# Performance work log

Measured on AMD Instinct MI355X. Metric: run time of the kernel, lower is better.

Reference implementation:

```python
import jax, jax.numpy as jnp
import numpy as np
from jax import lax


def setup_inputs() -> dict:
    key = jax.random.key(0)
    x = jax.random.normal(key, (16, 3, 1024, 1024), dtype=jnp.float32)
    return {"x": x, "kernel_size": 7}


def _box_conv(x, kernel, pad):
    # x: (B,1,H,W), kernel: (1,1,k,k); 'same' spatial conv
    return lax.conv_general_dilated(
        x, kernel,
        window_strides=(1, 1),
        padding=[(pad, pad), (pad, pad)],
        dimension_numbers=("NCHW", "OIHW", "NCHW"),
    )


def reference(x, kernel_size):
    k = kernel_size
    pad = k // 2
    # ConvertToLuminance: for 4D input, x.dim()==4 -> channel mean (not RGB weights)
    lum = jnp.mean(x, axis=1, keepdims=True)  # (B,1,H,W)
    kernel = jnp.ones((1, 1, k, k), dtype=x.dtype) / (k * k)
    mean = _box_conv(lum, kernel, pad)
    sqr_mean = _box_conv(lum * lum, kernel, pad)
    var = sqr_mean - mean * mean
    return var
```

## Files before the change

### kernel.cpp

```cpp
#include <hip/hip_runtime.h>

#define Wd 1024
#define Hd 1024
#define SH 16
#define ITER (SH + 6)

__global__ __launch_bounds__(256, 4)
void lvm_stream(const float* __restrict__ x, float* __restrict__ out) {
    __shared__ __align__(16) float L[2][Wd + 8];

    const int b    = blockIdx.y;
    const int row0 = blockIdx.x * SH;
    const int tid  = threadIdx.x;
    const int c0   = tid * 4;

    const float* x0 = x + (size_t)b * 3 * Hd * Wd;
    const float* x1 = x0 + (size_t)Hd * Wd;
    const float* x2 = x1 + (size_t)Hd * Wd;
    float*       ob = out + (size_t)b * Hd * Wd;

    if (tid < 4) {
        L[0][tid] = 0.f; L[0][Wd + 4 + tid] = 0.f;
        L[1][tid] = 0.f; L[1][Wd + 4 + tid] = 0.f;
    }

    float4 ring1[7], ring2[7];

#pragma unroll
    for (int i = 0; i < ITER; ++i) {
        const int ri = row0 - 3 + i;
        float4 lum4 = make_float4(0.f, 0.f, 0.f, 0.f);
        if (ri >= 0 && ri < Hd) {
            size_t o = (size_t)ri * Wd + c0;
            float4 a = *(const float4*)(x0 + o);
            float4 g = *(const float4*)(x1 + o);
            float4 c = *(const float4*)(x2 + o);
            lum4.x = (a.x + g.x + c.x) * (1.f / 3.f);
            lum4.y = (a.y + g.y + c.y) * (1.f / 3.f);
            lum4.z = (a.z + g.z + c.z) * (1.f / 3.f);
            lum4.w = (a.w + g.w + c.w) * (1.f / 3.f);
        }
        float* Lr = L[i & 1];
        *(float4*)(Lr + 4 + c0) = lum4;
        __syncthreads();

        float4 va = *(const float4*)(Lr + c0);
        float4 vb = *(const float4*)(Lr + c0 + 4);
        float4 vc = *(const float4*)(Lr + c0 + 8);
        float v1 = va.y, v2 = va.z, v3 = va.w;
        float v4 = vb.x, v5 = vb.y, v6 = vb.z, v7 = vb.w;
        float v8 = vc.x, v9 = vc.y, v10 = vc.z;

        float s1a = v1 + v2 + v3 + v4 + v5 + v6 + v7;
        float s1b = s1a - v1 + v8;
        float s1c = s1b - v2 + v9;
        float s1d = s1c - v3 + v10;

        float q1 = v1 * v1, q2 = v2 * v2, q3 = v3 * v3, q4 = v4 * v4;
        float q5 = v5 * v5, q6 = v6 * v6, q7 = v7 * v7, q8 = v8 * v8;
        float q9 = v9 * v9, q10 = v10 * v10;
        float s2a = q1 + q2 + q3 + q4 + q5 + q6 + q7;
        float s2b = s2a - q1 + q8;
        float s2c = s2b - q2 + q9;
        float s2d = s2c - q3 + q10;

        ring1[i % 7] = make_float4(s1a, s1b, s1c, s1d);
        ring2[i % 7] = make_float4(s2a, s2b, s2c, s2d);

        if (i >= 6) {
            float4 t1 = ring1[0], t2 = ring2[0];
#pragma unroll
            for (int k = 1; k < 7; ++k) {
                t1.x += ring1[k].x; t1.y += ring1[k].y;
                t1.z += ring1[k].z; t1.w += ring1[k].w;
                t2.x += ring2[k].x; t2.y += ring2[k].y;
                t2.z += ring2[k].z; t2.w += ring2[k].w;
            }
            const float inv = 1.f / 49.f;
            float4 r;
            float mx = t1.x * inv, my = t1.y * inv, mz = t1.z * inv, mw = t1.w * inv;
            r.x = t2.x * inv - mx * mx;
            r.y = t2.y * inv - my * my;
            r.z = t2.z * inv - mz * mz;
            r.w = t2.w * inv - mw * mw;
            const int ro = row0 + i - 6;
            *(float4*)(ob + (size_t)ro * Wd + c0) = r;
        }
    }
}

extern "C" void kernel_launch(void* const* d_in, const int* in_sizes, int n_in,
                              void* d_out, int out_size, void* d_ws, size_t ws_size,
                              hipStream_t stream) {
    const float* x = (const float*)d_in[0];
    float* out = (float*)d_out;
    dim3 grid(Hd / SH, 16);
    lvm_stream<<<grid, dim3(256), 0, stream>>>(x, out);
}
```

Before: 301.9 us.

## Replace LDS halo exchange with wavefront shuffles and double row strip height

Horizontal neighbors now come from wavefront shuffles instead of a shared-memory row buffer, which removes the per-row __syncthreads barrier. Wavefront edge lanes reload the adjacent float4 from global memory to fill the halo. The strip height grows from 16 to 32 rows, cutting redundant halo-row reads, and output stores become nontemporal. The trade-offs are extra global loads at wave boundaries, more unrolled code, and half as many blocks.

```diff
diff --git a/kernel.cpp b/kernel.cpp
--- a/kernel.cpp
+++ b/kernel.cpp
@@ -1,17 +1,27 @@
 #include <hip/hip_runtime.h>
+
+typedef float f4 __attribute__((ext_vector_type(4)));
 
 #define Wd 1024
 #define Hd 1024
-#define SH 16
+#define SH 32
 #define ITER (SH + 6)
+
+__device__ __forceinline__ f4 load_lum(const float* __restrict__ x0,
+                                       const float* __restrict__ x1,
+                                       const float* __restrict__ x2, size_t o) {
+    f4 a = *(const f4*)(x0 + o);
+    f4 g = *(const f4*)(x1 + o);
+    f4 c = *(const f4*)(x2 + o);
+    return (a + g + c) * (1.f / 3.f);
+}
 
 __global__ __launch_bounds__(256, 4)
 void lvm_stream(const float* __restrict__ x, float* __restrict__ out) {
-    __shared__ __align__(16) float L[2][Wd + 8];
-
     const int b    = blockIdx.y;
     const int row0 = blockIdx.x * SH;
     const int tid  = threadIdx.x;
+    const int lane = tid & 63;
     const int c0   = tid * 4;
 
     const float* x0 = x + (size_t)b * 3 * Hd * Wd;
@@ -19,37 +29,38 @@
     const float* x2 = x1 + (size_t)Hd * Wd;
     float*       ob = out + (size_t)b * Hd * Wd;
 
-    if (tid < 4) {
-        L[0][tid] = 0.f; L[0][Wd + 4 + tid] = 0.f;
-        L[1][tid] = 0.f; L[1][Wd + 4 + tid] = 0.f;
-    }
-
-    float4 ring1[7], ring2[7];
+    f4 ring1[7], ring2[7];
 
 #pragma unroll
     for (int i = 0; i < ITER; ++i) {
         const int ri = row0 - 3 + i;
-        float4 lum4 = make_float4(0.f, 0.f, 0.f, 0.f);
-        if (ri >= 0 && ri < Hd) {
-            size_t o = (size_t)ri * Wd + c0;
-            float4 a = *(const float4*)(x0 + o);
-            float4 g = *(const float4*)(x1 + o);
-            float4 c = *(const float4*)(x2 + o);
-            lum4.x = (a.x + g.x + c.x) * (1.f / 3.f);
-            lum4.y = (a.y + g.y + c.y) * (1.f / 3.f);
-            lum4.z = (a.z + g.z + c.z) * (1.f / 3.f);
-            lum4.w = (a.w + g.w + c.w) * (1.f / 3.f);
+        const bool rv = (ri >= 0) && (ri < Hd);
+        f4 lum = {0.f, 0.f, 0.f, 0.f};
+        if (rv) lum = load_lum(x0, x1, x2, (size_t)ri * Wd + c0);
+
+        float v1  = __shfl_up(lum.y, 1);
+        float v2  = __shfl_up(lum.z, 1);
+        float v3  = __shfl_up(lum.w, 1);
+        float v8  = __shfl_down(lum.x, 1);
+        float v9  = __shfl_down(lum.y, 1);
+        float v10 = __shfl_down(lum.z, 1);
+
+        if (lane == 0) {
+            v1 = v2 = v3 = 0.f;
+            if (rv && c0 >= 4) {
+                f4 e = load_lum(x0, x1, x2, (size_t)ri * Wd + (c0 - 4));
+                v1 = e.y; v2 = e.z; v3 = e.w;
+            }
         }
-        float* Lr = L[i & 1];
-        *(float4*)(Lr + 4 + c0) = lum4;
-        __syncthreads();
+        if (lane == 63) {
+            v8 = v9 = v10 = 0.f;
+            if (rv && (c0 + 4) < Wd) {
+                f4 e = load_lum(x0, x1, x2, (size_t)ri * Wd + (c0 + 4));
+                v8 = e.x; v9 = e.y; v10 = e.z;
+            }
+        }
 
-        float4 va = *(const float4*)(Lr + c0);
-        float4 vb = *(const float4*)(Lr + c0 + 4);
-        float4 vc = *(const float4*)(Lr + c0 + 8);
-        float v1 = va.y, v2 = va.z, v3 = va.w;
-        float v4 = vb.x, v5 = vb.y, v6 = vb.z, v7 = vb.w;
-        float v8 = vc.x, v9 = vc.y, v10 = vc.z;
+        const float v4 = lum.x, v5 = lum.y, v6 = lum.z, v7 = lum.w;
 
         float s1a = v1 + v2 + v3 + v4 + v5 + v6 + v7;
         float s1b = s1a - v1 + v8;
@@ -64,27 +75,18 @@
         float s2c = s2b - q2 + q9;
         float s2d = s2c - q3 + q10;
 
-        ring1[i % 7] = make_float4(s1a, s1b, s1c, s1d);
-        ring2[i % 7] = make_float4(s2a, s2b, s2c, s2d);
+        ring1[i % 7] = (f4){s1a, s1b, s1c, s1d};
+        ring2[i % 7] = (f4){s2a, s2b, s2c, s2d};
 
         if (i >= 6) {
-            float4 t1 = ring1[0], t2 = ring2[0];
+            f4 t1 = ring1[0], t2 = ring2[0];
 #pragma unroll
-            for (int k = 1; k < 7; ++k) {
-                t1.x += ring1[k].x; t1.y += ring1[k].y;
-                t1.z += ring1[k].z; t1.w += ring1[k].w;
-                t2.x += ring2[k].x; t2.y += ring2[k].y;
-                t2.z += ring2[k].z; t2.w += ring2[k].w;
-            }
+            for (int k = 1; k < 7; ++k) { t1 += ring1[k]; t2 += ring2[k]; }
             const float inv = 1.f / 49.f;
-            float4 r;
-            float mx = t1.x * inv, my = t1.y * inv, mz = t1.z * inv, mw = t1.w * inv;
-            r.x = t2.x * inv - mx * mx;
-            r.y = t2.y * inv - my * my;
-            r.z = t2.z * inv - mz * mz;
-            r.w = t2.w * inv - mw * mw;
+            f4 m = t1 * inv;
+            f4 r = t2 * inv - m * m;
             const int ro = row0 + i - 6;
-            *(float4*)(ob + (size_t)ro * Wd + c0) = r;
+            __builtin_nontemporal_store(r, (f4*)(ob + (size_t)ro * Wd + c0));
         }
     }
 }
```

New measurement: 319.0 us. 5.7% more time.
